# Performance work log

Measured on AMD Instinct MI355X. Metric: run time of the kernel, lower is better.

## Reference

```python
import jax, jax.numpy as jnp
import numpy as np

EMBED_DIM = 1024
NUM_HEADS = 16
HEAD_DIM = EMBED_DIM // NUM_HEADS
SCALE = HEAD_DIM ** -0.5


def setup_inputs() -> dict:
    key = jax.random.key(0)
    ks = jax.random.split(key, 11)
    b, n, c = 2, 2048, EMBED_DIM
    # xavier_uniform bound for square [c, c] weight
    bound = float(np.sqrt(6.0 / (c + c)))
    def xavier(k):
        return jax.random.uniform(k, (c, c), jnp.float32, -bound, bound)
    return {
        "q": jax.random.normal(ks[0], (b, n, c), jnp.float32),
        "k": jax.random.normal(ks[1], (b, n, c), jnp.float32),
        "v": jax.random.normal(ks[2], (b, n, c), jnp.float32),
        "wq": xavier(ks[3]), "bq": jnp.zeros((c,), jnp.float32),
        "wk": xavier(ks[4]), "bk": jnp.zeros((c,), jnp.float32),
        "wv": xavier(ks[5]), "bv": jnp.zeros((c,), jnp.float32),
        "wo": xavier(ks[6]), "bo": jnp.zeros((c,), jnp.float32),
    }


def reference(q, k, v, wq, bq, wk, bk, wv, bv, wo, bo):
    b, n, c = q.shape
    h, d = NUM_HEADS, HEAD_DIM
    # linear projections (torch Linear: x @ W^T + b)
    qh = (q @ wq.T + bq).reshape(b, n, h, d).transpose(0, 2, 1, 3)  # b h n d
    kh = (k @ wk.T + bk).reshape(b, n, h, d).transpose(0, 2, 1, 3)
    vh = (v @ wv.T + bv).reshape(b, n, h, d).transpose(0, 2, 1, 3)
    dots = jnp.einsum('bhid,bhjd->bhij', qh, kh) * SCALE
    attn = jax.nn.softmax(dots, axis=-1)  # dropout p=0 -> identity
    out = jnp.einsum('bhij,bhjd->bhid', attn, vh)
    out = out.transpose(0, 2, 1, 3).reshape(b, n, c)
    return out @ wo.T + bo
```

## Files before the change

kernel.cpp:

```cpp
#include <hip/hip_runtime.h>


typedef float f32x4 __attribute__((ext_vector_type(4)));
typedef float f32x16 __attribute__((ext_vector_type(16)));
typedef __bf16 bf16x8 __attribute__((ext_vector_type(8)));

#define SEQ 2048
#define CH 1024
#define NH 16
#define HD 64
#define TOK 4096
#define QSCALE 0.18033688011112042f

__device__ __forceinline__ unsigned short f2b(float f) {
  unsigned int u = __float_as_uint(f);
  u = (u + 0x7FFFu + ((u >> 16) & 1u)) >> 16;
  return (unsigned short)u;
}

__device__ __forceinline__ float fexp2(float x) {
  float r;
  asm("v_exp_f32 %0, %1" : "=v"(r) : "v"(x));
  return r;
}

__device__ __forceinline__ unsigned int cvtpk(float lo, float hi) {
  unsigned int r;
  asm("v_cvt_pk_bf16_f32 %0, %1, %2" : "=v"(r) : "v"(lo), "v"(hi));
  return r;
}

__device__ __forceinline__ void gload16(const void* g, void* l) {
  __builtin_amdgcn_global_load_lds(
      (const __attribute__((address_space(1))) unsigned int*)g,
      (__attribute__((address_space(3))) unsigned int*)l, 16, 0, 0);
}

struct CvtArgs {
  const float* src[7];
  unsigned short* dst[7];
  int n4[7];
};

__global__ __launch_bounds__(256) void cvt_kernel(CvtArgs a) {
  const int s = blockIdx.y;
  const int n4 = a.n4[s];
  const float4* __restrict__ src = (const float4*)a.src[s];
  unsigned short* __restrict__ dst = a.dst[s];
  const int stride = gridDim.x * blockDim.x;
  for (int i = blockIdx.x * blockDim.x + threadIdx.x; i < n4; i += stride) {
    float4 w = src[i];
    ushort4 o;
    o.x = f2b(w.x); o.y = f2b(w.y); o.z = f2b(w.z); o.w = f2b(w.w);
    *(ushort4*)(dst + 4 * (size_t)i) = o;
  }
}

struct ProjArgs {
  const unsigned short* X[2];
  const unsigned short* W[2];
  const float* bias[2];
  unsigned short* outb[2];
  float* outf;
  int mode[2];
};

__device__ __forceinline__ void proj_stage(
    const unsigned short* __restrict__ X, const unsigned short* __restrict__ W,
    int mt, int nt, int k0, unsigned char* buf, int wid, int lane) {
#pragma unroll
  for (int is = 0; is < 2; ++is) {
    const int p = (wid * 2 + is) * 1024 + lane * 16;
    gload16(X + (size_t)(mt * 128 + (p >> 6)) * CH + k0 + ((p & 63) >> 1),
            buf + (wid * 2 + is) * 1024);
  }
  {
    const int p = wid * 1024 + lane * 16;
    gload16(W + (size_t)(nt * 64 + (p >> 6)) * CH + k0 + ((p & 63) >> 1),
            buf + 8192 + wid * 1024);
  }
}

__global__ __launch_bounds__(256, 4) void proj_kernel(ProjArgs a) {
  constexpr int BUFB = 8192 + 4096;
  __shared__ __align__(16) unsigned char smem[3 * BUFB];
  const int z = blockIdx.z;
  const unsigned short* __restrict__ X = a.X[z];
  const unsigned short* __restrict__ W = a.W[z];
  const float* __restrict__ bias = a.bias[z];
  unsigned short* __restrict__ outb = a.outb[z];
  float* __restrict__ outf = a.outf;
  const int mode = a.mode[z];
  const int tid = threadIdx.x, wid = tid >> 6, lane = tid & 63;
  const int wm = wid >> 1, wn = wid & 1;
  const int mt = blockIdx.x, nt = blockIdx.y;
  const int l15 = lane & 15, l4 = lane >> 4;

  float bvv[2];
#pragma unroll
  for (int nj = 0; nj < 2; ++nj)
    bvv[nj] = bias[nt * 64 + wn * 32 + nj * 16 + l15];

  f32x4 acc[4][2] = {};

  proj_stage(X, W, mt, nt, 0, smem, wid, lane);
  proj_stage(X, W, mt, nt, 32, smem + BUFB, wid, lane);

  for (int s = 0; s < 32; ++s) {
    if (s < 31) asm volatile("s_waitcnt vmcnt(3)" ::: "memory");
    else        asm volatile("s_waitcnt vmcnt(0)" ::: "memory");
    __builtin_amdgcn_s_barrier();
    __builtin_amdgcn_sched_barrier(0);
    if (s + 2 < 32)
      proj_stage(X, W, mt, nt, (s + 2) * 32, smem + ((s + 2) % 3) * BUFB, wid, lane);

    unsigned char* Al = smem + (s % 3) * BUFB;
    unsigned char* Bl = Al + 8192;
    bf16x8 af[4], bfr[2];
#pragma unroll
    for (int mi = 0; mi < 4; ++mi)
      af[mi] = *(const bf16x8*)(Al + (wm * 64 + mi * 16 + l15) * 64 + l4 * 16);
#pragma unroll
    for (int nj = 0; nj < 2; ++nj)
      bfr[nj] = *(const bf16x8*)(Bl + (wn * 32 + nj * 16 + l15) * 64 + l4 * 16);
    __builtin_amdgcn_s_setprio(1);
#pragma unroll
    for (int mi = 0; mi < 4; ++mi)
#pragma unroll
      for (int nj = 0; nj < 2; ++nj)
        acc[mi][nj] = __builtin_amdgcn_mfma_f32_16x16x32_bf16(af[mi], bfr[nj], acc[mi][nj], 0, 0, 0);
    __builtin_amdgcn_s_setprio(0);
  }

  const int row0 = mt * 128 + wm * 64;
  const int col0 = nt * 64 + wn * 32;
#pragma unroll
  for (int nj = 0; nj < 2; ++nj) {
    const int col = col0 + nj * 16 + l15;
    const float bv = bvv[nj];
    const int h = col >> 6, d = col & 63;
    if (mode == 3) {
#pragma unroll
      for (int mi = 0; mi < 4; ++mi) {
        const int row = row0 + mi * 16 + l4 * 4;
        const int b = row >> 11, n = row & (SEQ - 1);
        ushort4 o;
        o.x = f2b(acc[mi][nj][0] + bv);
        o.y = f2b(acc[mi][nj][1] + bv);
        o.z = f2b(acc[mi][nj][2] + bv);
        o.w = f2b(acc[mi][nj][3] + bv);
        *(ushort4*)(outb + ((size_t)(b * NH + h) * HD + d) * SEQ + n) = o;
      }
    } else {
#pragma unroll
      for (int mi = 0; mi < 4; ++mi) {
#pragma unroll
        for (int r = 0; r < 4; ++r) {
          const int row = row0 + mi * 16 + l4 * 4 + r;
          float v = acc[mi][nj][r] + bv;
          if (mode == 0) v *= QSCALE;
          if (mode == 2) {
            outf[(size_t)row * CH + col] = v;
          } else {
            const int b = row >> 11, n = row & (SEQ - 1);
            outb[(((size_t)(b * NH + h) * SEQ + n) << 6) + d] = f2b(v);
          }
        }
      }
    }
  }
}

__device__ __forceinline__ void stage_kv(
    const unsigned short* __restrict__ Kb, const unsigned short* __restrict__ Vb,
    int j0, unsigned char* buf, int ws3, int lane) {
#pragma unroll
  for (int is = 0; is < 2; ++is) {
    const int p = ws3 * 2048 + is * 1024 + lane * 16;
    const int row = p >> 7;
    const int sw = ((p & 127) ^ ((row & 7) << 4)) >> 1;
    gload16(Kb + (size_t)(j0 + row) * HD + sw, buf + ws3 * 2048 + is * 1024);
    gload16(Vb + (size_t)row * SEQ + j0 + sw, buf + 8192 + ws3 * 2048 + is * 1024);
  }
}

__global__ __launch_bounds__(512, 4) void attn_kernel(
    const unsigned short* __restrict__ Qh, const unsigned short* __restrict__ Kh,
    const unsigned short* __restrict__ Vt, unsigned short* __restrict__ AO) {
  __shared__ __align__(16) unsigned char smem[81920];
  const int tid = threadIdx.x, wid = tid >> 6, lane = tid & 63;
  const int l31 = lane & 31, h = lane >> 5;
  const int grp = wid >> 2, wq = wid & 3;
  const int bid = blockIdx.x;
  const int swz = (bid & 7) * 64 + (bid >> 3);
  const int qt = swz & 15, bh = swz >> 4;

  const unsigned short* Qb = Qh + ((size_t)bh * SEQ + qt * 128) * HD;
  const unsigned short* Kb = Kh + (size_t)bh * SEQ * HD;
  const unsigned short* Vb = Vt + (size_t)bh * HD * SEQ;
  unsigned char* kvb = smem + grp * 32768;
  unsigned char* Qreg = smem + 65536;
  const int jbase = grp * 16;

#pragma unroll
  for (int is = 0; is < 4; ++is) {
    const int p = wq * 4096 + is * 1024 + lane * 16;
    const int row = p >> 7;
    const int sw = ((p & 127) ^ ((row & 7) << 4)) >> 1;
    gload16(Qb + (size_t)row * HD + sw, Qreg + wq * 4096 + is * 1024);
  }
  stage_kv(Kb, Vb, jbase * 64, kvb, wq, lane);
  asm volatile("s_waitcnt vmcnt(4)" ::: "memory");

  bf16x8 qf[4];
  const int qrow = wq * 32 + l31;
#pragma unroll
  for (int ks = 0; ks < 4; ++ks)
    qf[ks] = *(const bf16x8*)(Qreg + qrow * 128 +
                              ((ks * 32 + h * 16) ^ ((qrow & 7) << 4)));

  stage_kv(Kb, Vb, (jbase + 1) * 64, kvb + 16384, wq, lane);

  f32x16 O[2] = {};
  float m = -1e30f, l = 0.f;

  for (int it = 0; it < 16; ++it) {
    if (it < 15) asm volatile("s_waitcnt vmcnt(4)" ::: "memory");
    else         asm volatile("s_waitcnt vmcnt(0)" ::: "memory");
    __builtin_amdgcn_s_barrier();
    __builtin_amdgcn_sched_barrier(0);

    unsigned char* Kc = kvb + ((it & 1) << 14);
    unsigned char* Vc = Kc + 8192;

    f32x16 st[2] = {};
    __builtin_amdgcn_s_setprio(1);
#pragma unroll
    for (int kb = 0; kb < 2; ++kb) {
#pragma unroll
      for (int ks = 0; ks < 4; ++ks) {
        const int krow = kb * 32 + l31;
        const bf16x8 kf = *(const bf16x8*)(Kc + krow * 128 +
                                           ((ks * 32 + h * 16) ^ ((krow & 7) << 4)));
        st[kb] = __builtin_amdgcn_mfma_f32_32x32x16_bf16(kf, qf[ks], st[kb], 0, 0, 0);
      }
    }
    __builtin_amdgcn_s_setprio(0);

    float t[8];
#pragma unroll
    for (int i = 0; i < 8; ++i)
      t[i] = fmaxf(fmaxf(st[0][i], st[0][i + 8]), fmaxf(st[1][i], st[1][i + 8]));
#pragma unroll
    for (int i = 0; i < 4; ++i) t[i] = fmaxf(t[i], t[i + 4]);
    float pmax = fmaxf(fmaxf(t[0], t[1]), fmaxf(t[2], t[3]));
    pmax = fmaxf(pmax, __shfl_xor(pmax, 32));
    if (__any(pmax > m + 8.f)) {
      const float mnew = fmaxf(m, pmax);
      const float alpha = fexp2(m - mnew);
#pragma unroll
      for (int r = 0; r < 16; ++r) {
        const int qO = (r & 3) + 8 * (r >> 2) + 4 * h;
        const float aO = __shfl(alpha, qO);
        O[0][r] *= aO;
        O[1][r] *= aO;
      }
      l *= alpha;
      m = mnew;
    }
#pragma unroll
    for (int kb = 0; kb < 2; ++kb)
#pragma unroll
      for (int i = 0; i < 16; ++i) st[kb][i] = fexp2(st[kb][i] - m);
    float s[8];
#pragma unroll
    for (int i = 0; i < 8; ++i)
      s[i] = (st[0][i] + st[0][i + 8]) + (st[1][i] + st[1][i + 8]);
#pragma unroll
    for (int i = 0; i < 4; ++i) s[i] += s[i + 4];
    float rs = (s[0] + s[1]) + (s[2] + s[3]);
    rs += __shfl_xor(rs, 32);
    l += rs;

    unsigned int pk[2][8];
#pragma unroll
    for (int kb = 0; kb < 2; ++kb)
#pragma unroll
      for (int j = 0; j < 8; ++j)
        pk[kb][j] = cvtpk(st[kb][2 * j], st[kb][2 * j + 1]);

    __builtin_amdgcn_s_setprio(1);
#pragma unroll
    for (int kk = 0; kk < 4; ++kk) {
      const int kb = kk >> 1, j0 = (kk & 1) * 4;
      const unsigned int p0 = pk[kb][j0 + 0], p1 = pk[kb][j0 + 1];
      const unsigned int p2 = pk[kb][j0 + 2], p3 = pk[kb][j0 + 3];
      const unsigned int u0 = h ? p0 : p2;
      const unsigned int u1 = h ? p1 : p3;
      const unsigned int su0 = __shfl_xor(u0, 32);
      const unsigned int su1 = __shfl_xor(u1, 32);
      const unsigned int d0 = h ? su0 : p0;
      const unsigned int d1 = h ? su1 : p1;
      const unsigned int d2 = h ? p2 : su0;
      const unsigned int d3 = h ? p3 : su1;
      uint4 aw = make_uint4(d0, d1, d2, d3);
      const bf16x8 af = *(const bf16x8*)&aw;
#pragma unroll
      for (int db = 0; db < 2; ++db) {
        const int vrow = db * 32 + l31;
        const bf16x8 vf = *(const bf16x8*)(Vc + vrow * 128 +
                                           ((kk * 32 + h * 16) ^ ((vrow & 7) << 4)));
        O[db] = __builtin_amdgcn_mfma_f32_32x32x16_bf16(af, vf, O[db], 0, 0, 0);
      }
    }
    __builtin_amdgcn_s_setprio(0);

    __builtin_amdgcn_s_barrier();
    if (it + 2 < 16)
      stage_kv(Kb, Vb, (jbase + it + 2) * 64, Kc, wq, lane);
  }

  float2* slotO = (float2*)(smem + wq * 8960);
  float2* slotML = (float2*)(smem + wq * 8960 + 8704);
  if (grp == 1) {
    float2* dst = slotO + lane * 17;
#pragma unroll
    for (int i = 0; i < 8; ++i) dst[i] = make_float2(O[0][2 * i], O[0][2 * i + 1]);
#pragma unroll
    for (int i = 0; i < 8; ++i) dst[8 + i] = make_float2(O[1][2 * i], O[1][2 * i + 1]);
    if (h == 0) slotML[l31] = make_float2(m, l);
  }
  __builtin_amdgcn_s_barrier();
  if (grp == 0) {
    const float* src = (const float*)(slotO + lane * 17);
    const float2 ml1 = slotML[l31];
    const float mm = fmaxf(m, ml1.x);
    const float a0 = fexp2(m - mm), a1 = fexp2(ml1.x - mm);
    const float inv = 1.f / (a0 * l + a1 * ml1.y);
    const float w0 = a0 * inv, w1 = a1 * inv;
    const int b = bh >> 4, hh = bh & 15;
#pragma unroll
    for (int r = 0; r < 16; ++r) {
      const int qO = (r & 3) + 8 * (r >> 2) + 4 * h;
      const float s0 = __shfl(w0, qO), s1 = __shfl(w1, qO);
      const int n = qt * 128 + wq * 32 + qO;
      const size_t base = ((size_t)(b * SEQ + n)) * CH + hh * HD;
      AO[base + l31] = f2b(O[0][r] * s0 + src[r] * s1);
      AO[base + 32 + l31] = f2b(O[1][r] * s0 + src[16 + r] * s1);
    }
  }
}

extern "C" void kernel_launch(void* const* d_in, const int* in_sizes, int n_in,
                              void* d_out, int out_size, void* d_ws, size_t ws_size,
                              hipStream_t stream) {
  (void)in_sizes; (void)n_in; (void)out_size; (void)ws_size;
  const float* q  = (const float*)d_in[0];
  const float* k  = (const float*)d_in[1];
  const float* v  = (const float*)d_in[2];
  const float* wq = (const float*)d_in[3];
  const float* bq = (const float*)d_in[4];
  const float* wk = (const float*)d_in[5];
  const float* bk = (const float*)d_in[6];
  const float* wv = (const float*)d_in[7];
  const float* bv = (const float*)d_in[8];
  const float* wo = (const float*)d_in[9];
  const float* bo = (const float*)d_in[10];

  unsigned char* ws = (unsigned char*)d_ws;
  const size_t MB8 = 8u << 20;
  unsigned short* qb  = (unsigned short*)(ws + 0 * MB8);
  unsigned short* kb  = (unsigned short*)(ws + 1 * MB8);
  unsigned short* vb  = (unsigned short*)(ws + 2 * MB8);
  unsigned short* wqb = (unsigned short*)(ws + 3 * MB8);
  unsigned short* wkb = (unsigned short*)(ws + 3 * MB8 + 1 * 2097152);
  unsigned short* wvb = (unsigned short*)(ws + 3 * MB8 + 2 * 2097152);
  unsigned short* wob = (unsigned short*)(ws + 3 * MB8 + 3 * 2097152);
  unsigned short* Qh  = (unsigned short*)(ws + 4 * MB8);
  unsigned short* Kh  = (unsigned short*)(ws + 5 * MB8);
  unsigned short* VtT = kb;
  unsigned short* AO  = qb;
  float* out = (float*)d_out;

  CvtArgs ca;
  ca.src[0] = q;  ca.dst[0] = qb;  ca.n4[0] = TOK * CH / 4;
  ca.src[1] = k;  ca.dst[1] = kb;  ca.n4[1] = TOK * CH / 4;
  ca.src[2] = v;  ca.dst[2] = vb;  ca.n4[2] = TOK * CH / 4;
  ca.src[3] = wq; ca.dst[3] = wqb; ca.n4[3] = CH * CH / 4;
  ca.src[4] = wk; ca.dst[4] = wkb; ca.n4[4] = CH * CH / 4;
  ca.src[5] = wv; ca.dst[5] = wvb; ca.n4[5] = CH * CH / 4;
  ca.src[6] = wo; ca.dst[6] = wob; ca.n4[6] = CH * CH / 4;
  cvt_kernel<<<dim3(1024, 7), 256, 0, stream>>>(ca);

  ProjArgs qk;
  qk.X[0] = qb;  qk.W[0] = wqb; qk.bias[0] = bq; qk.outb[0] = Qh; qk.mode[0] = 0;
  qk.X[1] = kb;  qk.W[1] = wkb; qk.bias[1] = bk; qk.outb[1] = Kh; qk.mode[1] = 1;
  qk.outf = nullptr;
  proj_kernel<<<dim3(32, 16, 2), 256, 0, stream>>>(qk);

  ProjArgs vp;
  vp.X[0] = vb;  vp.W[0] = wvb; vp.bias[0] = bv; vp.outb[0] = VtT; vp.mode[0] = 3;
  vp.X[1] = vb;  vp.W[1] = wvb; vp.bias[1] = bv; vp.outb[1] = VtT; vp.mode[1] = 3;
  vp.outf = nullptr;
  proj_kernel<<<dim3(32, 16, 1), 256, 0, stream>>>(vp);

  attn_kernel<<<dim3(512), 512, 0, stream>>>(Qh, Kh, VtT, AO);

  ProjArgs op;
  op.X[0] = AO; op.W[0] = wob; op.bias[0] = bo; op.outb[0] = nullptr; op.mode[0] = 2;
  op.X[1] = AO; op.W[1] = wob; op.bias[1] = bo; op.outb[1] = nullptr; op.mode[1] = 2;
  op.outf = out;
  proj_kernel<<<dim3(32, 16, 1), 256, 0, stream>>>(op);
}
```

Baseline: 134.4 us.

## Fuse fp32-to-bf16 activation conversion into QKV projection and merge V launch

The QKV projection now reads fp32 activations straight from the inputs, converts them to bf16 in registers and writes them to shared memory, so the separate conversion pass over q, k and v is dropped. Only the weights still go through the conversion kernel. Q, K and V projections run in one launch (grid z=3), and the output projection gets its own specialized kernel. This removes a full fp32 read and bf16 write/read round trip of the activations plus one launch, at the cost of a more complex software pipeline with register-staged A loads and hand-tuned waitcnts.

```diff
diff --git a/kernel.cpp b/kernel.cpp
--- a/kernel.cpp
+++ b/kernel.cpp
@@ -37,9 +37,9 @@
 }
 
 struct CvtArgs {
-  const float* src[7];
-  unsigned short* dst[7];
-  int n4[7];
+  const float* src[4];
+  unsigned short* dst[4];
+  int n4[4];
 };
 
 __global__ __launch_bounds__(256) void cvt_kernel(CvtArgs a) {
@@ -56,81 +56,107 @@
   }
 }
 
-struct ProjArgs {
-  const unsigned short* X[2];
-  const unsigned short* W[2];
-  const float* bias[2];
-  unsigned short* outb[2];
-  float* outf;
-  int mode[2];
+struct Proj3Args {
+  const float* X[3];
+  const unsigned short* W[3];
+  const float* bias[3];
+  unsigned short* outb[3];
+  int mode[3];
 };
 
-__device__ __forceinline__ void proj_stage(
-    const unsigned short* __restrict__ X, const unsigned short* __restrict__ W,
-    int mt, int nt, int k0, unsigned char* buf, int wid, int lane) {
-#pragma unroll
-  for (int is = 0; is < 2; ++is) {
-    const int p = (wid * 2 + is) * 1024 + lane * 16;
-    gload16(X + (size_t)(mt * 128 + (p >> 6)) * CH + k0 + ((p & 63) >> 1),
-            buf + (wid * 2 + is) * 1024);
-  }
-  {
-    const int p = wid * 1024 + lane * 16;
-    gload16(W + (size_t)(nt * 64 + (p >> 6)) * CH + k0 + ((p & 63) >> 1),
-            buf + 8192 + wid * 1024);
-  }
-}
-
-__global__ __launch_bounds__(256, 4) void proj_kernel(ProjArgs a) {
+__global__ __launch_bounds__(256, 4) void proj3_kernel(Proj3Args a) {
   constexpr int BUFB = 8192 + 4096;
   __shared__ __align__(16) unsigned char smem[3 * BUFB];
   const int z = blockIdx.z;
-  const unsigned short* __restrict__ X = a.X[z];
+  const float* __restrict__ X = a.X[z];
   const unsigned short* __restrict__ W = a.W[z];
   const float* __restrict__ bias = a.bias[z];
   unsigned short* __restrict__ outb = a.outb[z];
-  float* __restrict__ outf = a.outf;
   const int mode = a.mode[z];
   const int tid = threadIdx.x, wid = tid >> 6, lane = tid & 63;
   const int wm = wid >> 1, wn = wid & 1;
   const int mt = blockIdx.x, nt = blockIdx.y;
   const int l15 = lane & 15, l4 = lane >> 4;
 
+  const float* Asrc = X + (size_t)(mt * 128 + (tid >> 1)) * CH + (tid & 1) * 16;
+  const unsigned short* Bsrc = W + (size_t)(nt * 64 + (tid >> 2)) * CH + (tid & 3) * 8;
+  unsigned char* const Adst0 = smem + tid * 32;
+  unsigned char* const Bdst0 = smem + 8192 + tid * 16;
+
   float bvv[2];
 #pragma unroll
   for (int nj = 0; nj < 2; ++nj)
     bvv[nj] = bias[nt * 64 + wn * 32 + nj * 16 + l15];
 
   f32x4 acc[4][2] = {};
-
-  proj_stage(X, W, mt, nt, 0, smem, wid, lane);
-  proj_stage(X, W, mt, nt, 32, smem + BUFB, wid, lane);
-
-  for (int s = 0; s < 32; ++s) {
-    if (s < 31) asm volatile("s_waitcnt vmcnt(3)" ::: "memory");
-    else        asm volatile("s_waitcnt vmcnt(0)" ::: "memory");
-    __builtin_amdgcn_s_barrier();
-    __builtin_amdgcn_sched_barrier(0);
-    if (s + 2 < 32)
-      proj_stage(X, W, mt, nt, (s + 2) * 32, smem + ((s + 2) % 3) * BUFB, wid, lane);
-
-    unsigned char* Al = smem + (s % 3) * BUFB;
-    unsigned char* Bl = Al + 8192;
-    bf16x8 af[4], bfr[2];
-#pragma unroll
-    for (int mi = 0; mi < 4; ++mi)
-      af[mi] = *(const bf16x8*)(Al + (wm * 64 + mi * 16 + l15) * 64 + l4 * 16);
-#pragma unroll
-    for (int nj = 0; nj < 2; ++nj)
-      bfr[nj] = *(const bf16x8*)(Bl + (wn * 32 + nj * 16 + l15) * 64 + l4 * 16);
-    __builtin_amdgcn_s_setprio(1);
-#pragma unroll
-    for (int mi = 0; mi < 4; ++mi)
-#pragma unroll
-      for (int nj = 0; nj < 2; ++nj)
-        acc[mi][nj] = __builtin_amdgcn_mfma_f32_16x16x32_bf16(af[mi], bfr[nj], acc[mi][nj], 0, 0, 0);
-    __builtin_amdgcn_s_setprio(0);
-  }
+  float4 a0[4], a1[4];
+
+#define LOADA(SET, T)                                                        \
+  {                                                                          \
+    _Pragma("unroll") for (int j = 0; j < 4; ++j)                            \
+        SET[j] = *(const float4*)(Asrc + (T) * 32 + 4 * j);                  \
+  }
+#define DMAB(T) gload16(Bsrc + (T) * 32, Bdst0 + ((T) % 3) * BUFB);
+#define WRITEA(SET, T)                                                       \
+  {                                                                          \
+    unsigned int pk[8];                                                      \
+    _Pragma("unroll") for (int j = 0; j < 4; ++j) {                          \
+      pk[2 * j] = cvtpk(SET[j].x, SET[j].y);                                 \
+      pk[2 * j + 1] = cvtpk(SET[j].z, SET[j].w);                             \
+    }                                                                        \
+    unsigned char* d = Adst0 + ((T) % 3) * BUFB;                             \
+    *(uint4*)d = make_uint4(pk[0], pk[1], pk[2], pk[3]);                     \
+    *(uint4*)(d + 16) = make_uint4(pk[4], pk[5], pk[6], pk[7]);              \
+  }
+
+  LOADA(a0, 0);
+  DMAB(0);
+  LOADA(a1, 1);
+  DMAB(1);
+  asm volatile("s_waitcnt vmcnt(6)" ::: "memory");
+  WRITEA(a0, 0);
+  LOADA(a0, 2);
+  asm volatile("s_waitcnt vmcnt(5)" ::: "memory");
+  WRITEA(a1, 1);
+
+#define STEP(S, WSET, LSET)                                                  \
+  {                                                                          \
+    const int s_ = (S);                                                      \
+    asm volatile("s_waitcnt lgkmcnt(0)" ::: "memory");                       \
+    __builtin_amdgcn_s_barrier();                                            \
+    __builtin_amdgcn_sched_barrier(0);                                       \
+    if (s_ + 2 < 32) DMAB(s_ + 2);                                           \
+    if (s_ + 3 < 32) LOADA(LSET, s_ + 3);                                    \
+    if (s_ <= 28)                                                            \
+      asm volatile("s_waitcnt vmcnt(5)" ::: "memory");                       \
+    else if (s_ == 29)                                                       \
+      asm volatile("s_waitcnt vmcnt(1)" ::: "memory");                       \
+    else                                                                     \
+      asm volatile("s_waitcnt vmcnt(0)" ::: "memory");                       \
+    if (s_ + 2 < 32) WRITEA(WSET, s_ + 2);                                   \
+    unsigned char* Al = smem + (s_ % 3) * BUFB;                              \
+    unsigned char* Bl = Al + 8192;                                           \
+    bf16x8 af[4], bfr[2];                                                    \
+    _Pragma("unroll") for (int mi = 0; mi < 4; ++mi)                         \
+        af[mi] = *(const bf16x8*)(Al + (wm * 64 + mi * 16 + l15) * 64 + l4 * 16); \
+    _Pragma("unroll") for (int nj = 0; nj < 2; ++nj)                         \
+        bfr[nj] = *(const bf16x8*)(Bl + (wn * 32 + nj * 16 + l15) * 64 + l4 * 16); \
+    __builtin_amdgcn_s_setprio(1);                                           \
+    _Pragma("unroll") for (int mi = 0; mi < 4; ++mi)                         \
+        _Pragma("unroll") for (int nj = 0; nj < 2; ++nj)                     \
+        acc[mi][nj] = __builtin_amdgcn_mfma_f32_16x16x32_bf16(af[mi], bfr[nj], \
+                                                              acc[mi][nj], 0, 0, 0); \
+    __builtin_amdgcn_s_setprio(0);                                           \
+  }
+
+  for (int s2 = 0; s2 < 32; s2 += 2) {
+    STEP(s2, a0, a1);
+    STEP(s2 + 1, a1, a0);
+  }
+#undef STEP
+#undef LOADA
+#undef DMAB
+#undef WRITEA
 
   const int row0 = mt * 128 + wm * 64;
   const int col0 = nt * 64 + wn * 32;
@@ -159,15 +185,87 @@
           const int row = row0 + mi * 16 + l4 * 4 + r;
           float v = acc[mi][nj][r] + bv;
           if (mode == 0) v *= QSCALE;
-          if (mode == 2) {
-            outf[(size_t)row * CH + col] = v;
-          } else {
-            const int b = row >> 11, n = row & (SEQ - 1);
-            outb[(((size_t)(b * NH + h) * SEQ + n) << 6) + d] = f2b(v);
-          }
+          const int b = row >> 11, n = row & (SEQ - 1);
+          outb[(((size_t)(b * NH + h) * SEQ + n) << 6) + d] = f2b(v);
         }
       }
     }
+  }
+}
+
+__device__ __forceinline__ void projo_stage(
+    const unsigned short* __restrict__ X, const unsigned short* __restrict__ W,
+    int mt, int nt, int k0, unsigned char* buf, int wid, int lane) {
+#pragma unroll
+  for (int is = 0; is < 2; ++is) {
+    const int p = (wid * 2 + is) * 1024 + lane * 16;
+    gload16(X + (size_t)(mt * 128 + (p >> 6)) * CH + k0 + ((p & 63) >> 1),
+            buf + (wid * 2 + is) * 1024);
+  }
+  {
+    const int p = wid * 1024 + lane * 16;
+    gload16(W + (size_t)(nt * 64 + (p >> 6)) * CH + k0 + ((p & 63) >> 1),
+            buf + 8192 + wid * 1024);
+  }
+}
+
+__global__ __launch_bounds__(256, 4) void projo_kernel(
+    const unsigned short* __restrict__ X, const unsigned short* __restrict__ W,
+    const float* __restrict__ bias, float* __restrict__ outf) {
+  constexpr int BUFB = 8192 + 4096;
+  __shared__ __align__(16) unsigned char smem[3 * BUFB];
+  const int tid = threadIdx.x, wid = tid >> 6, lane = tid & 63;
+  const int wm = wid >> 1, wn = wid & 1;
+  const int mt = blockIdx.x, nt = blockIdx.y;
+  const int l15 = lane & 15, l4 = lane >> 4;
+
+  float bvv[2];
+#pragma unroll
+  for (int nj = 0; nj < 2; ++nj)
+    bvv[nj] = bias[nt * 64 + wn * 32 + nj * 16 + l15];
+
+  f32x4 acc[4][2] = {};
+
+  projo_stage(X, W, mt, nt, 0, smem, wid, lane);
+  projo_stage(X, W, mt, nt, 32, smem + BUFB, wid, lane);
+
+  for (int s = 0; s < 32; ++s) {
+    if (s < 31) asm volatile("s_waitcnt vmcnt(3)" ::: "memory");
+    else        asm volatile("s_waitcnt vmcnt(0)" ::: "memory");
+    __builtin_amdgcn_s_barrier();
+    __builtin_amdgcn_sched_barrier(0);
+    if (s + 2 < 32)
+      projo_stage(X, W, mt, nt, (s + 2) * 32, smem + ((s + 2) % 3) * BUFB, wid, lane);
+
+    unsigned char* Al = smem + (s % 3) * BUFB;
+    unsigned char* Bl = Al + 8192;
+    bf16x8 af[4], bfr[2];
+#pragma unroll
+    for (int mi = 0; mi < 4; ++mi)
+      af[mi] = *(const bf16x8*)(Al + (wm * 64 + mi * 16 + l15) * 64 + l4 * 16);
+#pragma unroll
+    for (int nj = 0; nj < 2; ++nj)
+      bfr[nj] = *(const bf16x8*)(Bl + (wn * 32 + nj * 16 + l15) * 64 + l4 * 16);
+    __builtin_amdgcn_s_setprio(1);
+#pragma unroll
+    for (int mi = 0; mi < 4; ++mi)
+#pragma unroll
+      for (int nj = 0; nj < 2; ++nj)
+        acc[mi][nj] = __builtin_amdgcn_mfma_f32_16x16x32_bf16(af[mi], bfr[nj], acc[mi][nj], 0, 0, 0);
+    __builtin_amdgcn_s_setprio(0);
+  }
+
+  const int row0 = mt * 128 + wm * 64;
+  const int col0 = nt * 64 + wn * 32;
+#pragma unroll
+  for (int nj = 0; nj < 2; ++nj) {
+    const int col = col0 + nj * 16 + l15;
+    const float bv = bvv[nj];
+#pragma unroll
+    for (int mi = 0; mi < 4; ++mi)
+#pragma unroll
+      for (int r = 0; r < 4; ++r)
+        outf[(size_t)(row0 + mi * 16 + l4 * 4 + r) * CH + col] = acc[mi][nj][r] + bv;
   }
 }
 
@@ -369,46 +467,30 @@
 
   unsigned char* ws = (unsigned char*)d_ws;
   const size_t MB8 = 8u << 20;
-  unsigned short* qb  = (unsigned short*)(ws + 0 * MB8);
-  unsigned short* kb  = (unsigned short*)(ws + 1 * MB8);
-  unsigned short* vb  = (unsigned short*)(ws + 2 * MB8);
+  unsigned short* AO  = (unsigned short*)(ws + 0 * MB8);
+  unsigned short* Vt  = (unsigned short*)(ws + 1 * MB8);
   unsigned short* wqb = (unsigned short*)(ws + 3 * MB8);
   unsigned short* wkb = (unsigned short*)(ws + 3 * MB8 + 1 * 2097152);
   unsigned short* wvb = (unsigned short*)(ws + 3 * MB8 + 2 * 2097152);
   unsigned short* wob = (unsigned short*)(ws + 3 * MB8 + 3 * 2097152);
   unsigned short* Qh  = (unsigned short*)(ws + 4 * MB8);
   unsigned short* Kh  = (unsigned short*)(ws + 5 * MB8);
-  unsigned short* VtT = kb;
-  unsigned short* AO  = qb;
   float* out = (float*)d_out;
 
   CvtArgs ca;
-  ca.src[0] = q;  ca.dst[0] = qb;  ca.n4[0] = TOK * CH / 4;
-  ca.src[1] = k;  ca.dst[1] = kb;  ca.n4[1] = TOK * CH / 4;
-  ca.src[2] = v;  ca.dst[2] = vb;  ca.n4[2] = TOK * CH / 4;
-  ca.src[3] = wq; ca.dst[3] = wqb; ca.n4[3] = CH * CH / 4;
-  ca.src[4] = wk; ca.dst[4] = wkb; ca.n4[4] = CH * CH / 4;
-  ca.src[5] = wv; ca.dst[5] = wvb; ca.n4[5] = CH * CH / 4;
-  ca.src[6] = wo; ca.dst[6] = wob; ca.n4[6] = CH * CH / 4;
-  cvt_kernel<<<dim3(1024, 7), 256, 0, stream>>>(ca);
-
-  ProjArgs qk;
-  qk.X[0] = qb;  qk.W[0] = wqb; qk.bias[0] = bq; qk.outb[0] = Qh; qk.mode[0] = 0;
-  qk.X[1] = kb;  qk.W[1] = wkb; qk.bias[1] = bk; qk.outb[1] = Kh; qk.mode[1] = 1;
-  qk.outf = nullptr;
-  proj_kernel<<<dim3(32, 16, 2), 256, 0, stream>>>(qk);
-
-  ProjArgs vp;
-  vp.X[0] = vb;  vp.W[0] = wvb; vp.bias[0] = bv; vp.outb[0] = VtT; vp.mode[0] = 3;
-  vp.X[1] = vb;  vp.W[1] = wvb; vp.bias[1] = bv; vp.outb[1] = VtT; vp.mode[1] = 3;
-  vp.outf = nullptr;
-  proj_kernel<<<dim3(32, 16, 1), 256, 0, stream>>>(vp);
-
-  attn_kernel<<<dim3(512), 512, 0, stream>>>(Qh, Kh, VtT, AO);
-
-  ProjArgs op;
-  op.X[0] = AO; op.W[0] = wob; op.bias[0] = bo; op.outb[0] = nullptr; op.mode[0] = 2;
-  op.X[1] = AO; op.W[1] = wob; op.bias[1] = bo; op.outb[1] = nullptr; op.mode[1] = 2;
-  op.outf = out;
-  proj_kernel<<<dim3(32, 16, 1), 256, 0, stream>>>(op);
-}
+  ca.src[0] = wq; ca.dst[0] = wqb; ca.n4[0] = CH * CH / 4;
+  ca.src[1] = wk; ca.dst[1] = wkb; ca.n4[1] = CH * CH / 4;
+  ca.src[2] = wv; ca.dst[2] = wvb; ca.n4[2] = CH * CH / 4;
+  ca.src[3] = wo; ca.dst[3] = wob; ca.n4[3] = CH * CH / 4;
+  cvt_kernel<<<dim3(512, 4), 256, 0, stream>>>(ca);
+
+  Proj3Args p3;
+  p3.X[0] = q; p3.W[0] = wqb; p3.bias[0] = bq; p3.outb[0] = Qh; p3.mode[0] = 0;
+  p3.X[1] = k; p3.W[1] = wkb; p3.bias[1] = bk; p3.outb[1] = Kh; p3.mode[1] = 1;
+  p3.X[2] = v; p3.W[2] = wvb; p3.bias[2] = bv; p3.outb[2] = Vt; p3.mode[2] = 3;
+  proj3_kernel<<<dim3(32, 16, 3), 256, 0, stream>>>(p3);
+
+  attn_kernel<<<dim3(512), 512, 0, stream>>>(Qh, Kh, Vt, AO);
+
+  projo_kernel<<<dim3(32, 16), 256, 0, stream>>>(AO, wob, bo, out);
+}
```

After: 144.6 us. 7.6% more time.
